# Kernel optimization log

Hardware: AMD Instinct MI355X
Metric: run time of the kernel (lower is better)

Reference implementation:

```python
import jax, jax.numpy as jnp
import numpy as np

K = 20          # k_neighbors from __init__
B, N = 4, 8192  # batch, points
EPS_NORM = 1e-12  # F.normalize eps


def setup_inputs() -> dict:
    key = jax.random.key(0)
    ks = jax.random.split(key, 4)
    point_cloud = jax.random.normal(ks[0], (B, N, 3), dtype=jnp.float32)
    vis_mask = jnp.ones((B, N), dtype=bool)

    def init_w(k, shape):
        return jax.random.normal(k, shape, dtype=jnp.float32) / np.sqrt(shape[1]).astype(np.float32)

    W1 = init_w(ks[1], (64, 10));  b1 = jnp.zeros((64,),  jnp.float32)
    W2 = init_w(ks[2], (128, 64)); b2 = jnp.zeros((128,), jnp.float32)
    W3 = init_w(ks[3], (256, 128)); b3 = jnp.zeros((256,), jnp.float32)
    return {"point_cloud": point_cloud, "vis_mask": vis_mask,
            "W1": W1, "b1": b1, "W2": W2, "b2": b2, "W3": W3, "b3": b3}


def _knn(points, k):
    # points: (B,N,3) -> knn_idx (B,N,k), excluding self (smallest distance)
    sq = jnp.sum(points * points, axis=-1)  # (B,N)
    d = sq[:, :, None] + sq[:, None, :] - 2.0 * jnp.einsum('bnd,bmd->bnm', points, points)
    _, idx = jax.lax.top_k(-d, k + 1)       # k+1 smallest distances
    return idx[:, :, 1:k + 1]


def _geometry(points, k):
    # local neighborhood features + PCA normals + curvature
    knn_idx = _knn(points, k)                              # (B,N,k)
    bidx = jnp.arange(points.shape[0])[:, None, None]
    neighbors = points[bidx, knn_idx]                      # (B,N,k,3)
    local = neighbors - points[:, :, None, :]              # (B,N,k,3)
    centered = local - jnp.mean(local, axis=2, keepdims=True)
    cov = jnp.einsum('bnki,bnkj->bnij', centered, centered)  # (B,N,3,3)
    w, v = jnp.linalg.eigh(cov)  # eigenvalues ascending
    # normal = eigenvector of smallest eigenvalue (== last right-singular vector of torch.svd)
    normals = v[..., :, 0]                                 # (B,N,3)
    dot = jnp.sum(normals * (-points), axis=-1, keepdims=True)
    normals = jnp.where(dot < 0, -normals, normals)
    normals = normals / jnp.maximum(jnp.linalg.norm(normals, axis=-1, keepdims=True), EPS_NORM)
    curvature = (w[..., 0] / (jnp.sum(w, axis=-1) + 1e-10))[..., None]  # (B,N,1)
    return local, normals, curvature


def reference(point_cloud, vis_mask, W1, b1, W2, b2, W3, b3):
    # vis_mask is all-True (equal visible count per batch required by source reshape)
    visible = jnp.where(vis_mask[..., None], point_cloud, 0.0)  # (B,N,3)
    local, normals, curvature = _geometry(visible, K)
    combined = jnp.concatenate(
        [visible, normals, curvature, jnp.mean(local, axis=2)], axis=-1)  # (B,N,10)
    # 1x1 Conv1d stack == pointwise MLP
    h = jax.nn.relu(jnp.einsum('bnc,oc->bno', combined, W1) + b1)
    h = jax.nn.relu(jnp.einsum('bnc,oc->bno', h, W2) + b2)
    h = jnp.einsum('bnc,oc->bno', h, W3) + b3
    return jnp.transpose(h, (0, 2, 1))  # (B,256,N)
```

## Files before the change

kernel.cpp:

```cpp
#include <hip/hip_runtime.h>
#include <stdint.h>

#define NPTS 8192
#define NBATCH 4
#define KNN_K 20
typedef unsigned long long ull;
typedef unsigned int uint;
typedef float v2f __attribute__((ext_vector_type(2)));

__device__ __forceinline__ v2f pk_fma(v2f a, v2f b, v2f c) {
  v2f d;
  asm("v_pk_fma_f32 %0, %1, %2, %3" : "=v"(d) : "v"(a), "v"(b), "v"(c));
  return d;
}
__device__ __forceinline__ v2f pk_mul(v2f a, v2f b) {
  v2f d;
  asm("v_pk_mul_f32 %0, %1, %2" : "=v"(d) : "v"(a), "v"(b));
  return d;
}

static constexpr int NBIN = 1024;
__device__ __forceinline__ int binof(float x) {
  int b = (int)floorf((x + 5.5f) * (1024.0f / 11.0f));
  return min(max(b, 0), NBIN - 1);
}

__global__ __launch_bounds__(256)
void zero_hist(uint* __restrict__ hist) {
  int g = blockIdx.x * 256 + threadIdx.x;
  if (g < NBATCH * NBIN) hist[g] = 0;
}

__global__ __launch_bounds__(256)
void prep_kernel(const float* __restrict__ pc, float4* __restrict__ p4,
                 uint* __restrict__ hist,
                 const float* __restrict__ W1, const float* __restrict__ W2,
                 const float* __restrict__ W3, float* __restrict__ T1,
                 float* __restrict__ T2, float* __restrict__ T3) {
  int g = blockIdx.x * 256 + threadIdx.x;
  if (g < NBATCH * NPTS) {
    float x = pc[g * 3 + 0], y = pc[g * 3 + 1], z = pc[g * 3 + 2];
    p4[g] = make_float4(x, y, z, fmaf(z, z, fmaf(y, y, x * x)));
    atomicAdd(&hist[(g >> 13) * NBIN + binof(x)], 1u);
  }
  if (g < 640) {
    T1[(g % 10) * 64 + g / 10] = W1[g];
  } else if (g < 640 + 8192) {
    int q = g - 640;
    T2[(q % 64) * 128 + q / 64] = W2[q];
  } else if (g < 640 + 8192 + 32768) {
    int q = g - 8832;
    T3[(q % 128) * 256 + q / 128] = W3[q];
  }
}

__global__ __launch_bounds__(1024)
void scan_kernel(const uint* __restrict__ hist, uint* __restrict__ offv,
                 uint* __restrict__ cursor) {
  const int b = blockIdx.x;
  const int t = threadIdx.x;
  __shared__ uint buf[2][NBIN];
  uint cnt = hist[b * NBIN + t];
  buf[0][t] = cnt;
  __syncthreads();
  int src = 0;
#pragma unroll
  for (int off = 1; off < NBIN; off <<= 1) {
    uint v = buf[src][t];
    if (t >= off) v += buf[src][t - off];
    buf[src ^ 1][t] = v;
    __syncthreads();
    src ^= 1;
  }
  uint inc = buf[src][t];
  uint exc = inc - cnt;
  offv[b * (NBIN + 1) + t] = exc;
  cursor[b * NBIN + t]     = exc;
  if (t == NBIN - 1) offv[b * (NBIN + 1) + NBIN] = inc;
}

__global__ __launch_bounds__(256)
void scatter_kernel(const float4* __restrict__ p4, uint* __restrict__ cursor,
                    float4* __restrict__ p4s, uint* __restrict__ o32) {
  int g = blockIdx.x * 256 + threadIdx.x;
  if (g >= NBATCH * NPTS) return;
  int b = g >> 13;
  float4 v = p4[g];
  uint pos = atomicAdd(&cursor[b * NBIN + binof(v.x)], 1u);
  p4s[(size_t)b * NPTS + pos] = v;
  o32[(size_t)b * NPTS + pos] = (uint)(g & (NPTS - 1));
}

static constexpr int ST   = 512;
static constexpr int RPW  = 4;
static constexpr int BR   = 16;
static constexpr int QCAP = 128;
static constexpr int TPAD = 66;

__global__ __launch_bounds__(256, 5)
void knn_kernel(const float4* __restrict__ p4s, const uint* __restrict__ o32,
                const uint* __restrict__ offv, int* __restrict__ knn_out) {
  const int tid  = threadIdx.x;
  const int lane = tid & 63;
  const int wv   = tid >> 6;
  const int row0 = blockIdx.x * BR + wv * RPW;
  const int bat  = row0 >> 13;
  const float4* __restrict__ Ps = p4s + (size_t)bat * NPTS;
  const uint*   __restrict__ Os = o32 + (size_t)bat * NPTS;
  const int rbase = row0 & (NPTS - 1);
  const int qrow0 = wv * RPW;

  __shared__ float plx[ST], ply[ST], plz[ST], plw[ST];
  __shared__ uint  qidx[BR][QCAP];
  __shared__ ull   kb2[4][4 * TPAD];
  __shared__ float thrv[4][RPW];
  __shared__ uint  qn[BR];
  __shared__ float wred[2][BR];
  __shared__ int   iwin[2];

  v2f rx2[RPW], ry2[RPW], rz2[RPW];
  float rqx[RPW], rpw[RPW];
#pragma unroll
  for (int r = 0; r < RPW; ++r) {
    float4 v = Ps[rbase + r];
    rx2[r] = (v2f){v.x, v.x};
    ry2[r] = (v2f){v.y, v.y};
    rz2[r] = (v2f){v.z, v.z};
    rqx[r] = v.x; rpw[r] = v.w;
  }
  const v2f m2 = {-2.0f, -2.0f};
  if (tid < BR) qn[tid] = 0;

#define STAGEW(base)                                                       \
  {                                                                        \
    float4 v = Ps[(base) + tid];                                           \
    plx[tid] = v.x; ply[tid] = v.y; plz[tid] = v.z; plw[tid] = v.w;        \
    v = Ps[(base) + tid + 256];                                            \
    plx[tid + 256] = v.x; ply[tid + 256] = v.y;                            \
    plz[tid + 256] = v.z; plw[tid + 256] = v.w;                            \
  }

  const int blk0 = (blockIdx.x * BR) & (NPTS - 1);
  const int c0   = min(max(blk0 + BR / 2 - 1024, 0), NPTS - 2048);

  float dmin[RPW];
#pragma unroll
  for (int r = 0; r < RPW; ++r) dmin[r] = __int_as_float(0x7f800000);

  for (int s = 0; s < 4; ++s) {
    __syncthreads();
    STAGEW(c0 + s * ST)
    __syncthreads();
#pragma unroll
    for (int tl = 0; tl < ST / 128; ++tl) {
      const int o = tl * 128 + 2 * lane;
      v2f x01 = *(const v2f*)&plx[o];
      v2f y01 = *(const v2f*)&ply[o];
      v2f z01 = *(const v2f*)&plz[o];
      v2f w01 = *(const v2f*)&plw[o];
#pragma unroll
      for (int r = 0; r < RPW; ++r) {
        v2f dot = pk_fma(rz2[r], z01, pk_fma(ry2[r], y01, pk_mul(rx2[r], x01)));
        v2f dp  = pk_fma(m2, dot, w01);
        dmin[r] = fminf(dmin[r], fminf(dp.x, dp.y));
      }
    }
  }

#pragma unroll
  for (int r = 0; r < RPW; ++r) {
    uint u  = __float_as_uint(dmin[r]);
    uint mk = u ^ (uint)(((int)u >> 31) | 0x80000000);
    kb2[wv][r * TPAD + lane] = ((ull)mk << 6) | (uint)lane;
  }
  __syncthreads();
  {
    const int rr = lane >> 4, jj = lane & 15;
    const ull* kp = &kb2[wv][rr * TPAD];
    ull e0 = kp[jj], e1 = kp[jj + 16], e2 = kp[jj + 32], e3 = kp[jj + 48];
    uint r0 = 0, r1 = 0, r2 = 0, r3 = 0;
    for (int i = 0; i < 64; ++i) {
      ull vi = kp[i];
      r0 += (uint)(vi < e0); r1 += (uint)(vi < e1);
      r2 += (uint)(vi < e2); r3 += (uint)(vi < e3);
    }
#define UNMAP(k) __uint_as_float(((uint)((k) >> 6)) ^ ((~((uint)((int)((uint)((k) >> 6)) >> 31))) | 0x80000000u))
    if (r0 == 20) thrv[wv][rr] = UNMAP(e0);
    if (r1 == 20) thrv[wv][rr] = UNMAP(e1);
    if (r2 == 20) thrv[wv][rr] = UNMAP(e2);
    if (r3 == 20) thrv[wv][rr] = UNMAP(e3);
#undef UNMAP
  }
  __syncthreads();
  float thr[RPW];
#pragma unroll
  for (int r = 0; r < RPW; ++r) thr[r] = thrv[wv][r] + 3e-5f;

  if (lane < RPW) {
    const int r = lane;
    float r2v = fmaxf(thr[r] + rpw[r], 0.0f);
    float rad = sqrtf(fmaf(r2v, 1.0001f, 1e-5f));
    wred[0][wv * RPW + r] = rqx[r] - rad - 1e-6f;
    wred[1][wv * RPW + r] = rqx[r] + rad + 1e-6f;
  }
  __syncthreads();
  if (tid == 0) {
    float lo = wred[0][0], hi = wred[1][0];
    for (int i = 1; i < BR; ++i) {
      lo = fminf(lo, wred[0][i]);
      hi = fmaxf(hi, wred[1][i]);
    }
    iwin[0] = (int)offv[bat * (NBIN + 1) + binof(lo)];
    iwin[1] = (int)offv[bat * (NBIN + 1) + binof(hi) + 1];
  }
  __syncthreads();
  const int wlo = iwin[0], whi = iwin[1];
  const int nst = (whi - wlo + ST - 1) / ST;

  for (int s = 0; s < nst; ++s) {
    __syncthreads();
    {
      int i0 = wlo + s * ST + tid;
      if (i0 < whi) {
        float4 v = Ps[i0];
        plx[tid] = v.x; ply[tid] = v.y; plz[tid] = v.z; plw[tid] = v.w;
      } else {
        plx[tid] = 0.0f; ply[tid] = 0.0f; plz[tid] = 0.0f;
        plw[tid] = __int_as_float(0x7f800000);
      }
      i0 += 256;
      if (i0 < whi) {
        float4 v = Ps[i0];
        plx[tid + 256] = v.x; ply[tid + 256] = v.y;
        plz[tid + 256] = v.z; plw[tid + 256] = v.w;
      } else {
        plx[tid + 256] = 0.0f; ply[tid + 256] = 0.0f; plz[tid + 256] = 0.0f;
        plw[tid + 256] = __int_as_float(0x7f800000);
      }
    }
    __syncthreads();
#pragma unroll
    for (int tl = 0; tl < ST / 128; ++tl) {
      const int o  = tl * 128 + 2 * lane;
      const int cb = wlo + s * ST + o;
      v2f x01 = *(const v2f*)&plx[o];
      v2f y01 = *(const v2f*)&ply[o];
      v2f z01 = *(const v2f*)&plz[o];
      v2f w01 = *(const v2f*)&plw[o];
#pragma unroll
      for (int r = 0; r < RPW; ++r) {
        v2f dot = pk_fma(rz2[r], z01, pk_fma(ry2[r], y01, pk_mul(rx2[r], x01)));
        v2f dp  = pk_fma(m2, dot, w01);
        if (dp.x <= thr[r]) {
          uint slot = atomicAdd(&qn[qrow0 + r], 1u);
          if (slot < QCAP) qidx[qrow0 + r][slot] = (uint)cb;
        }
        if (dp.y <= thr[r]) {
          uint slot = atomicAdd(&qn[qrow0 + r], 1u);
          if (slot < QCAP) qidx[qrow0 + r][slot] = (uint)(cb + 1);
        }
      }
    }
  }
  __syncthreads();

  for (int r = 0; r < RPW; ++r) {
    const float4 me = Ps[rbase + r];
    const uint orow = Os[rbase + r];
    const int cnt   = (int)(qn[qrow0 + r] < (uint)QCAP ? qn[qrow0 + r] : (uint)QCAP);

    ull k0 = ~0ull, k1 = ~0ull;
    uint i0 = 0, i1 = 0;
    if (lane < cnt) {
      uint si = qidx[qrow0 + r][lane];
      float4 Q  = Ps[si];
      i0 = Os[si];
      float dot = fmaf(me.z, Q.z, fmaf(me.y, Q.y, me.x * Q.x));
      float d   = fmaxf(fmaf(-2.0f, dot, me.w + Q.w), 0.0f);
      k0 = ((ull)__float_as_uint(d) << 32) | i0;
    }
    if (lane + 64 < cnt) {
      uint si = qidx[qrow0 + r][lane + 64];
      float4 Q  = Ps[si];
      i1 = Os[si];
      float dot = fmaf(me.z, Q.z, fmaf(me.y, Q.y, me.x * Q.x));
      float d   = fmaxf(fmaf(-2.0f, dot, me.w + Q.w), 0.0f);
      k1 = ((ull)__float_as_uint(d) << 32) | i1;
    }
    kb2[wv][lane]      = k0;
    kb2[wv][lane + 64] = k1;
    __syncthreads();

    uint r0 = 0, r1 = 0;
    for (int j = 0; j < cnt; ++j) {
      ull kj = kb2[wv][j];
      r0 += (uint)(kj < k0);
      r1 += (uint)(kj < k1);
    }
    const size_t obase = ((size_t)bat * NPTS + orow) * KNN_K;
    if (lane < cnt && r0 >= 1 && r0 <= 20) knn_out[obase + (r0 - 1)] = (int)i0;
    if (lane + 64 < cnt && r1 >= 1 && r1 <= 20) knn_out[obase + (r1 - 1)] = (int)i1;
    __syncthreads();
  }
#undef STAGEW
}

__global__ __launch_bounds__(256)
void geom_kernel(const float4* __restrict__ p4, const int* __restrict__ knn,
                 float* __restrict__ comb) {
  const int gid = blockIdx.x * 256 + threadIdx.x;
  if (gid >= NBATCH * NPTS) return;
  const int b = gid >> 13, n = gid & (NPTS - 1);
  const float4* __restrict__ P = p4 + (size_t)b * NPTS;
  const float4 me = P[n];
  const float px = me.x, py = me.y, pz = me.z;

  double sx = 0, sy = 0, sz = 0;
  double sxx = 0, sxy = 0, sxz = 0, syy = 0, syz = 0, szz = 0;
  const int* __restrict__ nb = knn + (size_t)gid * KNN_K;
#pragma unroll 4
  for (int k = 0; k < KNN_K; ++k) {
    float4 q = P[nb[k]];
    double qx = (double)q.x, qy = (double)q.y, qz = (double)q.z;
    sx += qx; sy += qy; sz += qz;
    sxx += qx * qx; sxy += qx * qy; sxz += qx * qz;
    syy += qy * qy; syz += qy * qz; szz += qz * qz;
  }
  const double mx = sx / KNN_K, my = sy / KNN_K, mz = sz / KNN_K;
  const double a00 = sxx - KNN_K * mx * mx;
  const double a01 = sxy - KNN_K * mx * my;
  const double a02 = sxz - KNN_K * mx * mz;
  const double a11 = syy - KNN_K * my * my;
  const double a12 = syz - KNN_K * my * mz;
  const double a22 = szz - KNN_K * mz * mz;

  const double qd = (a00 + a11 + a22) / 3.0;
  const double p1 = a01 * a01 + a02 * a02 + a12 * a12;
  const double d00 = a00 - qd, d11 = a11 - qd, d22 = a22 - qd;
  const double p2 = d00 * d00 + d11 * d11 + d22 * d22 + 2.0 * p1;

  double l0 = qd, l1 = qd, l2 = qd;
  double vx = 1.0, vy = 0.0, vz = 0.0;
  if (p2 > 0.0) {
    const double p  = sqrt(p2 / 6.0);
    const double ip = 1.0 / p;
    const double b00 = d00 * ip, b01 = a01 * ip, b02 = a02 * ip;
    const double b11 = d11 * ip, b12 = a12 * ip, b22 = d22 * ip;
    double detB = b00 * (b11 * b22 - b12 * b12)
                - b01 * (b01 * b22 - b12 * b02)
                + b02 * (b01 * b12 - b11 * b02);
    double r = 0.5 * detB;
    r = fmin(1.0, fmax(-1.0, r));
    const double phi = acos(r) / 3.0;
    l2 = qd + 2.0 * p * cos(phi);
    l0 = qd + 2.0 * p * cos(phi + 2.0943951023931953);
    l1 = 3.0 * qd - l0 - l2;

    const double m00 = a00 - l0, m11 = a11 - l0, m22 = a22 - l0;
    const double r0x = m00, r0y = a01, r0z = a02;
    const double r1x = a01, r1y = m11, r1z = a12;
    const double r2x = a02, r2y = a12, r2z = m22;
    double c0x = r0y * r1z - r0z * r1y, c0y = r0z * r1x - r0x * r1z, c0z = r0x * r1y - r0y * r1x;
    double c1x = r0y * r2z - r0z * r2y, c1y = r0z * r2x - r0x * r2z, c1z = r0x * r2y - r0y * r2x;
    double c2x = r1y * r2z - r1z * r2y, c2y = r1z * r2x - r1x * r2z, c2z = r1x * r2y - r1y * r2x;
    double n0 = c0x * c0x + c0y * c0y + c0z * c0z;
    double n1 = c1x * c1x + c1y * c1y + c1z * c1z;
    double n2 = c2x * c2x + c2y * c2y + c2z * c2z;
    double bx = c0x, by = c0y, bz = c0z, bn = n0;
    if (n1 > bn) { bx = c1x; by = c1y; bz = c1z; bn = n1; }
    if (n2 > bn) { bx = c2x; by = c2y; bz = c2z; bn = n2; }
    if (bn > 1e-300) {
      const double innv = 1.0 / sqrt(bn);
      vx = bx * innv; vy = by * innv; vz = bz * innv;
    }
  }
  const double dp = vx * (double)px + vy * (double)py + vz * (double)pz;
  if (dp > 0.0) { vx = -vx; vy = -vy; vz = -vz; }

  const double curv = l0 / (l0 + l1 + l2 + 1e-10);

  float o[10];
  o[0] = px; o[1] = py; o[2] = pz;
  o[3] = (float)vx; o[4] = (float)vy; o[5] = (float)vz;
  o[6] = (float)curv;
  o[7] = (float)(mx - (double)px);
  o[8] = (float)(my - (double)py);
  o[9] = (float)(mz - (double)pz);
#pragma unroll
  for (int i = 0; i < 10; ++i) comb[(size_t)gid * 10 + i] = o[i];
}

__global__ __launch_bounds__(256, 3)
void mlp_kernel(const float* __restrict__ comb,
                const float* __restrict__ wt1, const float* __restrict__ b1,
                const float* __restrict__ wt2, const float* __restrict__ b2,
                const float* __restrict__ wt3, const float* __restrict__ b3,
                float* __restrict__ out) {
  __shared__ float cmb[64][11];
  __shared__ float h1s[64][65];
  __shared__ float h2s[64][131];

  const int tid = threadIdx.x;
  const int p0  = blockIdx.x * 64;

  for (int i = tid; i < 640; i += 256) cmb[i / 10][i % 10] = comb[(size_t)p0 * 10 + i];
  __syncthreads();

  const int pt = tid & 63;
  const int wq = tid >> 6;

  {
    const int ob = __builtin_amdgcn_readfirstlane(wq * 16);
    v2f acc[8];
#pragma unroll
    for (int h = 0; h < 8; ++h) acc[h] = *(const v2f*)&b1[ob + 2 * h];
    for (int k = 0; k < 10; ++k) {
      float x = cmb[pt][k];
      v2f x2 = {x, x};
      const float* wrow = &wt1[k * 64 + ob];
#pragma unroll
      for (int h = 0; h < 8; ++h)
        acc[h] = pk_fma(*(const v2f*)&wrow[2 * h], x2, acc[h]);
    }
#pragma unroll
    for (int h = 0; h < 8; ++h) {
      h1s[pt][ob + 2 * h]     = fmaxf(acc[h].x, 0.0f);
      h1s[pt][ob + 2 * h + 1] = fmaxf(acc[h].y, 0.0f);
    }
  }
  __syncthreads();

  {
    const int ob = __builtin_amdgcn_readfirstlane(wq * 32);
    v2f acc[16];
#pragma unroll
    for (int h = 0; h < 16; ++h) acc[h] = *(const v2f*)&b2[ob + 2 * h];
    for (int k = 0; k < 64; ++k) {
      float x = h1s[pt][k];
      v2f x2 = {x, x};
      const float* wrow = &wt2[k * 128 + ob];
#pragma unroll
      for (int h = 0; h < 16; ++h)
        acc[h] = pk_fma(*(const v2f*)&wrow[2 * h], x2, acc[h]);
    }
#pragma unroll
    for (int h = 0; h < 16; ++h) {
      h2s[pt][ob + 2 * h]     = fmaxf(acc[h].x, 0.0f);
      h2s[pt][ob + 2 * h + 1] = fmaxf(acc[h].y, 0.0f);
    }
  }
  __syncthreads();

  {
    const int ob = __builtin_amdgcn_readfirstlane(wq * 64);
    v2f acc[32];
#pragma unroll
    for (int h = 0; h < 32; ++h) acc[h] = *(const v2f*)&b3[ob + 2 * h];
    for (int k = 0; k < 128; ++k) {
      float x = h2s[pt][k];
      v2f x2 = {x, x};
      const float* wrow = &wt3[k * 256 + ob];
#pragma unroll
      for (int h = 0; h < 32; ++h)
        acc[h] = pk_fma(*(const v2f*)&wrow[2 * h], x2, acc[h]);
    }
    const int gpt = p0 + pt;
    const int b = gpt >> 13, n = gpt & (NPTS - 1);
#pragma unroll
    for (int h = 0; h < 32; ++h) {
      out[((size_t)(b * 256 + ob + 2 * h)) * NPTS + n]     = acc[h].x;
      out[((size_t)(b * 256 + ob + 2 * h + 1)) * NPTS + n] = acc[h].y;
    }
  }
}

extern "C" void kernel_launch(void* const* d_in, const int* in_sizes, int n_in,
                              void* d_out, int out_size, void* d_ws, size_t ws_size,
                              hipStream_t stream) {
  const float* pc = (const float*)d_in[0];
  const float* W1 = (const float*)d_in[2];
  const float* b1 = (const float*)d_in[3];
  const float* W2 = (const float*)d_in[4];
  const float* b2 = (const float*)d_in[5];
  const float* W3 = (const float*)d_in[6];
  const float* b3 = (const float*)d_in[7];

  char* ws = (char*)d_ws;
  int*    knn  = (int*)(ws + 0);
  float4* p4   = (float4*)(ws + 2621440);
  float4* p4s  = (float4*)(ws + 3145728);
  uint*   o32  = (uint*)(ws + 3670016);
  uint*   hist = (uint*)(ws + 3801088);
  uint*   offv = (uint*)(ws + 3817472);
  uint*   curs = (uint*)(ws + 3833872);
  float*  wt1  = (float*)(ws + 3850256);
  float*  wt2  = (float*)(ws + 3852816);
  float*  wt3  = (float*)(ws + 3885584);
  float*  comb = (float*)(ws + 4016656);
  float*  outp = (float*)d_out;

  zero_hist<<<dim3(16), dim3(256), 0, stream>>>(hist);
  prep_kernel<<<dim3(163), dim3(256), 0, stream>>>(pc, p4, hist, W1, W2, W3,
                                                   wt1, wt2, wt3);
  scan_kernel<<<dim3(NBATCH), dim3(1024), 0, stream>>>(hist, offv, curs);
  scatter_kernel<<<dim3(128), dim3(256), 0, stream>>>(p4, curs, p4s, o32);
  knn_kernel<<<dim3(NBATCH * NPTS / BR), dim3(256), 0, stream>>>(p4s, o32, offv, knn);
  geom_kernel<<<dim3(NBATCH * NPTS / 256), dim3(256), 0, stream>>>(p4, knn, comb);
  mlp_kernel<<<dim3(NBATCH * NPTS / 64), dim3(256), 0, stream>>>(
      comb, wt1, b1, wt2, b2, wt3, b3, outp);
}
```

Before: 195.7 us.

## Register-tile MLP layers 2-3 over 4 points per thread with float4 stores

Layers 2 and 3 of the pointwise MLP now have each thread compute a 4-point by 8/16-channel register tile instead of one point across 32/64 channels. Each weight load is reused across four points, and the output is written as float4 vectors along the point dimension. Before, weights were read as wave-uniform scalar loads. Now the weight addresses differ by lane group, so they become per-lane vector loads. Occupancy is also lowered from 3 to 2 blocks per SIMD to leave room for more registers, and the LDS reads of h1s/h2s change to a strided pattern that may cause bank conflicts.

Measured after the change: 172.5 us (median of 2 runs). 11.9% less time.

```diff
diff --git a/kernel.cpp b/kernel.cpp
--- a/kernel.cpp
+++ b/kernel.cpp
@@ -390,7 +390,7 @@
   for (int i = 0; i < 10; ++i) comb[(size_t)gid * 10 + i] = o[i];
 }
 
-__global__ __launch_bounds__(256, 3)
+__global__ __launch_bounds__(256, 2)
 void mlp_kernel(const float* __restrict__ comb,
                 const float* __restrict__ wt1, const float* __restrict__ b1,
                 const float* __restrict__ wt2, const float* __restrict__ b2,
@@ -406,11 +406,9 @@
   for (int i = tid; i < 640; i += 256) cmb[i / 10][i % 10] = comb[(size_t)p0 * 10 + i];
   __syncthreads();
 
-  const int pt = tid & 63;
-  const int wq = tid >> 6;
-
   {
-    const int ob = __builtin_amdgcn_readfirstlane(wq * 16);
+    const int pt = tid & 63;
+    const int ob = (tid >> 6) * 16;
     v2f acc[8];
 #pragma unroll
     for (int h = 0; h < 8; ++h) acc[h] = *(const v2f*)&b1[ob + 2 * h];
@@ -430,46 +428,71 @@
   }
   __syncthreads();
 
+  const int pg = tid & 15;
+  const int og = tid >> 4;
+
   {
-    const int ob = __builtin_amdgcn_readfirstlane(wq * 32);
-    v2f acc[16];
-#pragma unroll
-    for (int h = 0; h < 16; ++h) acc[h] = *(const v2f*)&b2[ob + 2 * h];
+    const int ob = og * 8;
+    v2f acc[4][4];
+#pragma unroll
+    for (int h = 0; h < 4; ++h) {
+      v2f bv = *(const v2f*)&b2[ob + 2 * h];
+#pragma unroll
+      for (int i = 0; i < 4; ++i) acc[i][h] = bv;
+    }
     for (int k = 0; k < 64; ++k) {
-      float x = h1s[pt][k];
-      v2f x2 = {x, x};
       const float* wrow = &wt2[k * 128 + ob];
-#pragma unroll
-      for (int h = 0; h < 16; ++h)
-        acc[h] = pk_fma(*(const v2f*)&wrow[2 * h], x2, acc[h]);
-    }
-#pragma unroll
-    for (int h = 0; h < 16; ++h) {
-      h2s[pt][ob + 2 * h]     = fmaxf(acc[h].x, 0.0f);
-      h2s[pt][ob + 2 * h + 1] = fmaxf(acc[h].y, 0.0f);
-    }
+      v2f w[4];
+#pragma unroll
+      for (int h = 0; h < 4; ++h) w[h] = *(const v2f*)&wrow[2 * h];
+#pragma unroll
+      for (int i = 0; i < 4; ++i) {
+        float x = h1s[4 * pg + i][k];
+        v2f x2 = {x, x};
+#pragma unroll
+        for (int h = 0; h < 4; ++h) acc[i][h] = pk_fma(w[h], x2, acc[i][h]);
+      }
+    }
+#pragma unroll
+    for (int i = 0; i < 4; ++i)
+#pragma unroll
+      for (int h = 0; h < 4; ++h) {
+        h2s[4 * pg + i][ob + 2 * h]     = fmaxf(acc[i][h].x, 0.0f);
+        h2s[4 * pg + i][ob + 2 * h + 1] = fmaxf(acc[i][h].y, 0.0f);
+      }
   }
   __syncthreads();
 
   {
-    const int ob = __builtin_amdgcn_readfirstlane(wq * 64);
-    v2f acc[32];
-#pragma unroll
-    for (int h = 0; h < 32; ++h) acc[h] = *(const v2f*)&b3[ob + 2 * h];
+    const int ob = og * 16;
+    v2f acc[4][8];
+#pragma unroll
+    for (int h = 0; h < 8; ++h) {
+      v2f bv = *(const v2f*)&b3[ob + 2 * h];
+#pragma unroll
+      for (int i = 0; i < 4; ++i) acc[i][h] = bv;
+    }
     for (int k = 0; k < 128; ++k) {
-      float x = h2s[pt][k];
-      v2f x2 = {x, x};
       const float* wrow = &wt3[k * 256 + ob];
-#pragma unroll
-      for (int h = 0; h < 32; ++h)
-        acc[h] = pk_fma(*(const v2f*)&wrow[2 * h], x2, acc[h]);
-    }
-    const int gpt = p0 + pt;
-    const int b = gpt >> 13, n = gpt & (NPTS - 1);
-#pragma unroll
-    for (int h = 0; h < 32; ++h) {
-      out[((size_t)(b * 256 + ob + 2 * h)) * NPTS + n]     = acc[h].x;
-      out[((size_t)(b * 256 + ob + 2 * h + 1)) * NPTS + n] = acc[h].y;
+      v2f w[8];
+#pragma unroll
+      for (int h = 0; h < 8; ++h) w[h] = *(const v2f*)&wrow[2 * h];
+#pragma unroll
+      for (int i = 0; i < 4; ++i) {
+        float x = h2s[4 * pg + i][k];
+        v2f x2 = {x, x};
+#pragma unroll
+        for (int h = 0; h < 8; ++h) acc[i][h] = pk_fma(w[h], x2, acc[i][h]);
+      }
+    }
+    const int gpt = p0 + 4 * pg;
+    const int b = gpt >> 13, n0 = gpt & (NPTS - 1);
+#pragma unroll
+    for (int h = 0; h < 8; ++h) {
+      float4 v0 = make_float4(acc[0][h].x, acc[1][h].x, acc[2][h].x, acc[3][h].x);
+      float4 v1 = make_float4(acc[0][h].y, acc[1][h].y, acc[2][h].y, acc[3][h].y);
+      *(float4*)&out[((size_t)(b * 256 + ob + 2 * h)) * NPTS + n0]     = v0;
+      *(float4*)&out[((size_t)(b * 256 + ob + 2 * h + 1)) * NPTS + n0] = v1;
     }
   }
 }
```
